# Performance work log

Hardware: AMD Instinct MI355X
Metric: run time of the kernel (lower is better)

The kernel has to match this reference:

```python
import jax, jax.numpy as jnp
import numpy as np

CV_CHAN = 49  # displacement channels; radius = (CV_CHAN - 1) // 2 = 24


def conv1x1(x, W, b):
    # x: [B,C,H,Wd], W: [O,C], b: [O] -> [B,O,H,Wd]
    return jnp.einsum('oc,bchw->bohw', W, x) + b[None, :, None, None]


def corr_volume(f1, f2, radius, eps):
    """Shift-and-dot correlation along width. f1,f2: [B,C,H,W] -> [B,2r+1,H,W].
    Channel k corresponds to displacement d = k - radius; out-of-range positions are 0
    (handled by zero-padding, matching the torch zero-filled shifted tensors)."""
    f1n = f1 / (jnp.linalg.norm(f1, axis=1, keepdims=True) + eps)
    f2n = f2 / (jnp.linalg.norm(f2, axis=1, keepdims=True) + eps)
    Wd = f1.shape[3]
    pad = jnp.pad(f2n, ((0, 0), (0, 0), (0, 0), (radius, radius)))
    # shifted_k[x] = f2n[x - d] = pad[x + 2*radius - k]
    slices = [
        jnp.sum(f1n * jax.lax.dynamic_slice_in_dim(pad, 2 * radius - k, Wd, axis=3), axis=1)
        for k in range(2 * radius + 1)
    ]
    return jnp.stack(slices, axis=1)


def setup_inputs() -> dict:
    key = jax.random.key(0)
    ks = jax.random.split(key, 10)
    B, C, H, W = 4, 128, 128, 256
    F = 128  # fmap channels
    G = 96   # geo encoder output channels
    s = 0.05
    return {
        'feat_l1': jax.random.normal(ks[0], (B, C, H, W), jnp.float32),
        'feat_r1': jax.random.normal(ks[1], (B, C, H, W), jnp.float32),
        'cv0': jax.random.normal(ks[2], (B, CV_CHAN, H, W), jnp.float32),
        'cv1': jax.random.normal(ks[3], (B, CV_CHAN, H, W), jnp.float32),
        'cv2': jax.random.normal(ks[4], (B, CV_CHAN, H, W), jnp.float32),
        'W_f1': jax.random.normal(ks[5], (F, C), jnp.float32) * s,
        'b_f1': jnp.zeros((F,), jnp.float32),
        'W_f2': jax.random.normal(ks[6], (F, C), jnp.float32) * s,
        'b_f2': jnp.zeros((F,), jnp.float32),
        'W_geo': jax.random.normal(ks[7], (G, CV_CHAN), jnp.float32) * s,
        'b_geo': jnp.zeros((G,), jnp.float32),
        'W_sel': jax.random.normal(ks[8], (3, 3 * G), jnp.float32) * s,
        'b_sel': jnp.zeros((3,), jnp.float32),
    }


def reference(feat_l1, feat_r1, cv0, cv1, cv2,
              W_f1, b_f1, W_f2, b_f2, W_geo, b_geo, W_sel, b_sel):
    # init feature maps (init_fmap1 / init_fmap2 as 1x1 convs)
    fmap1 = conv1x1(feat_l1, W_f1, b_f1)
    fmap2 = conv1x1(feat_r1, W_f2, b_f2)
    radius = (CV_CHAN - 1) // 2
    init_corr = corr_volume(fmap1, fmap2, radius, 1e-8)  # [B, CV_CHAN, H, W]

    # geo_volume2 (1x1 conv CV_CHAN -> 96) applied to each geometric volume
    g0 = conv1x1(cv0, W_geo, b_geo)
    g1 = conv1x1(cv1, W_geo, b_geo)
    g2 = conv1x1(cv2, W_geo, b_geo)
    combined_g = jnp.concatenate([g0, g1, g2], axis=1)  # [B, 288, H, W]

    logits = conv1x1(combined_g, W_sel, b_sel)           # [B, 3, H, W]
    w = jax.nn.softmax(logits, axis=1)

    weighted = (w[:, 0:1] * cv0[:, :CV_CHAN]
                + w[:, 1:2] * cv1[:, :CV_CHAN]
                + w[:, 2:3] * cv2[:, :CV_CHAN])
    final = init_corr + weighted
    return (final, init_corr, w)
```

## Files before the change

### kernel.cpp

```cpp
#include <hip/hip_runtime.h>

#define HW 32768
#define WIDTH 256

typedef float f32x4 __attribute__((ext_vector_type(4)));
typedef short s16x8 __attribute__((ext_vector_type(8)));

__device__ __forceinline__ unsigned short f2bf(float f){
    unsigned int u = __float_as_uint(f);
    u += 0x7FFFu + ((u >> 16) & 1u);
    return (unsigned short)(u >> 16);
}
__device__ __forceinline__ unsigned int pk2(float a, float b){
    return (unsigned int)f2bf(a) | ((unsigned int)f2bf(b) << 16);
}

__global__ __launch_bounds__(256, 2) void k_fused(
    const float* __restrict__ fl, const float* __restrict__ fr,
    const float* __restrict__ W1, const float* __restrict__ W2,
    const float* __restrict__ b1, const float* __restrict__ b2,
    float* __restrict__ ic)
{
    __shared__ char pool[67584];
    __shared__ float s1[256], s2[256];
    unsigned short* Wlds = (unsigned short*)pool;
    unsigned short* f2s  = (unsigned short*)pool;
    float* G             = (float*)pool;

    const int blk  = blockIdx.x;
    const int b    = blk >> 7;
    const int h    = blk & 127;
    const int tid  = threadIdx.x;
    const int wv   = tid >> 6;
    const int lane = tid & 63;
    const int quad = lane >> 4;
    const int l15  = lane & 15;

    const float* feats[2] = { fl + (size_t)b * 128 * HW + h * WIDTH,
                              fr + (size_t)b * 128 * HW + h * WIDTH };
    const float* Wms[2]   = { W1, W2 };
    const float* bss[2]   = { b1, b2 };

    unsigned int f1p[64];

    #pragma unroll 1
    for (int F = 0; F < 2; ++F){
        const float* featB = feats[F];
        const float* Wm    = Wms[F];
        const float* bias  = bss[F];

        __syncthreads();
        {
            const int r = tid >> 1, c0 = (tid & 1) * 64;
            #pragma unroll
            for (int i = 0; i < 16; ++i){
                f32x4 v = *(const f32x4*)(Wm + r * 128 + c0 + i * 4);
                uint2 p; p.x = pk2(v[0], v[1]); p.y = pk2(v[2], v[3]);
                *(uint2*)&Wlds[r * 132 + c0 + i * 4] = p;
            }
        }
        __syncthreads();

        f32x4 acc[8][4];
        #pragma unroll
        for (int m = 0; m < 8; ++m)
            #pragma unroll
            for (int nt = 0; nt < 4; ++nt)
                acc[m][nt] = (f32x4){0.f, 0.f, 0.f, 0.f};

        float cur[8], nxt[8];
        {
            const float* bp = featB + (size_t)(quad * 8) * HW + wv * 64 + l15;
            #pragma unroll
            for (int j = 0; j < 8; ++j) cur[j] = bp[(size_t)j * HW];
        }

        #pragma unroll
        for (int kk = 0; kk < 4; ++kk){
            s16x8 af[8];
            #pragma unroll
            for (int m = 0; m < 8; ++m){
                const int base = (m * 16 + l15) * 132 + kk * 32 + quad * 8;
                union { uint2 q2[2]; s16x8 v; } r;
                r.q2[0] = *(const uint2*)&Wlds[base];
                r.q2[1] = *(const uint2*)&Wlds[base + 4];
                af[m] = r.v;
            }
            #pragma unroll
            for (int nt = 0; nt < 4; ++nt){
                const int kn  = kk + ((nt + 1) >> 2);
                const int ntn = (nt + 1) & 3;
                if (kn < 4){
                    const float* bp = featB + (size_t)(kn * 32 + quad * 8) * HW
                                      + wv * 64 + ntn * 16 + l15;
                    #pragma unroll
                    for (int j = 0; j < 8; ++j) nxt[j] = bp[(size_t)j * HW];
                }
                union { unsigned int u[4]; s16x8 v; } rb;
                rb.u[0] = pk2(cur[0], cur[1]); rb.u[1] = pk2(cur[2], cur[3]);
                rb.u[2] = pk2(cur[4], cur[5]); rb.u[3] = pk2(cur[6], cur[7]);
                #pragma unroll
                for (int m = 0; m < 8; ++m)
                    acc[m][nt] = __builtin_amdgcn_mfma_f32_16x16x32_bf16(af[m], rb.v, acc[m][nt], 0, 0, 0);
                #pragma unroll
                for (int j = 0; j < 8; ++j) cur[j] = nxt[j];
            }
        }

        float inv[4];
        #pragma unroll
        for (int nt = 0; nt < 4; ++nt){
            #pragma unroll
            for (int m = 0; m < 8; ++m)
                acc[m][nt] += *(const f32x4*)(bias + m * 16 + quad * 4);
            float n2 = 0.f;
            #pragma unroll
            for (int m = 0; m < 8; ++m)
                #pragma unroll
                for (int r = 0; r < 4; ++r)
                    n2 += acc[m][nt][r] * acc[m][nt][r];
            n2 += __shfl_xor(n2, 16, 64);
            n2 += __shfl_xor(n2, 32, 64);
            inv[nt] = 1.f / (sqrtf(n2) + 1e-8f);
        }

        if (F == 0){
            #pragma unroll
            for (int m = 0; m < 8; ++m)
                #pragma unroll
                for (int nt = 0; nt < 4; ++nt){
                    f1p[m * 8 + nt * 2 + 0] = pk2(acc[m][nt][0], acc[m][nt][1]);
                    f1p[m * 8 + nt * 2 + 1] = pk2(acc[m][nt][2], acc[m][nt][3]);
                }
            if (quad == 0){
                #pragma unroll
                for (int nt = 0; nt < 4; ++nt) s1[wv * 64 + nt * 16 + l15] = inv[nt];
            }
        } else {
            if (quad == 0){
                #pragma unroll
                for (int nt = 0; nt < 4; ++nt) s2[wv * 64 + nt * 16 + l15] = inv[nt];
            }
            __syncthreads();
            #pragma unroll
            for (int nt = 0; nt < 4; ++nt){
                const int px = wv * 64 + nt * 16 + l15;
                #pragma unroll
                for (int m = 0; m < 8; ++m){
                    uint2 p;
                    p.x = pk2(acc[m][nt][0], acc[m][nt][1]);
                    p.y = pk2(acc[m][nt][2], acc[m][nt][3]);
                    *(uint2*)&f2s[px * 132 + m * 16 + quad * 4] = p;
                }
            }
        }
    }
    __syncthreads();

    f32x4 acc_c[4][4];
    #pragma unroll
    for (int st = 0; st < 4; ++st)
        #pragma unroll
        for (int ct = 0; ct < 4; ++ct)
            acc_c[st][ct] = (f32x4){0.f, 0.f, 0.f, 0.f};

    #pragma unroll
    for (int st = 0; st < 4; ++st){
        s16x8 afc[4];
        #pragma unroll
        for (int kk = 0; kk < 4; ++kk){
            union { unsigned int u[4]; s16x8 v; } r;
            #pragma unroll
            for (int j2 = 0; j2 < 4; ++j2){
                const int rp  = j2 & 1;
                const int qs  = (quad & 1) * 2 + (j2 >> 1);
                const int src = qs * 16 + l15;
                unsigned int a0 = (unsigned int)__shfl((int)f1p[(kk * 2 + 0) * 8 + st * 2 + rp], src, 64);
                unsigned int a1 = (unsigned int)__shfl((int)f1p[(kk * 2 + 1) * 8 + st * 2 + rp], src, 64);
                r.u[j2] = (quad >> 1) ? a1 : a0;
            }
            afc[kk] = r.v;
        }
        #pragma unroll
        for (int ct = 0; ct < 4; ++ct){
            const int s = wv * 64 + st * 16 + ct * 16 + l15 - 24;
            const bool valid = (s >= 0) && (s < WIDTH);
            const int sc = valid ? s : 0;
            #pragma unroll
            for (int kk = 0; kk < 4; ++kk){
                union { uint2 q2[2]; s16x8 v; } rb;
                rb.q2[0] = *(const uint2*)&f2s[sc * 132 + kk * 32 + quad * 8];
                rb.q2[1] = *(const uint2*)&f2s[sc * 132 + kk * 32 + quad * 8 + 4];
                s16x8 bf = rb.v;
                if (!valid) bf = (s16x8){0,0,0,0,0,0,0,0};
                acc_c[st][ct] = __builtin_amdgcn_mfma_f32_16x16x32_bf16(afc[kk], bf, acc_c[st][ct], 0, 0, 0);
            }
        }
    }
    __syncthreads();
    #pragma unroll
    for (int st = 0; st < 4; ++st)
        #pragma unroll
        for (int ct = 0; ct < 4; ++ct)
            #pragma unroll
            for (int r = 0; r < 4; ++r)
                G[((wv * 4 + st) * 16 + quad * 4 + r) * 66 + ct * 16 + l15] = acc_c[st][ct][r];
    __syncthreads();

    float* obase = ic + (size_t)b * 49 * HW + (size_t)h * WIDTH;
    #pragma unroll
    for (int st = 0; st < 4; ++st){
        const int gx = wv * 64 + st * 16;
        const float sc1 = s1[gx + l15];
        const float* Grow = &G[((wv * 4 + st) * 16 + l15) * 66];
        #pragma unroll
        for (int i = 0; i < 13; ++i){
            const int dd = quad + i * 4;
            if (dd < 49){
                int s2i = gx + l15 + 24 - dd;
                s2i = s2i < 0 ? 0 : (s2i > 255 ? 255 : s2i);
                const float v = Grow[l15 + 48 - dd] * sc1 * s2[s2i];
                obase[(size_t)dd * HW + gx + l15] = v;
            }
        }
    }
}

__global__ void k_prep(const float* __restrict__ Wsel, const float* __restrict__ bsel,
                       const float* __restrict__ Wgeo, const float* __restrict__ bgeo,
                       float* __restrict__ M, float* __restrict__ c0)
{
    int u = threadIdx.x;
    if (u < 441){
        int s = u / 147; int r = u % 147; int i = r / 49; int k = r % 49;
        float acc = 0.f;
        for (int o = 0; o < 96; ++o)
            acc += Wsel[s * 288 + i * 96 + o] * Wgeo[o * 49 + k];
        M[u] = acc;
    } else if (u < 444){
        int s = u - 441;
        float acc = bsel[s];
        for (int i = 0; i < 3; ++i)
            for (int o = 0; o < 96; ++o)
                acc += Wsel[s * 288 + i * 96 + o] * bgeo[o];
        c0[s] = acc;
    }
}

__global__ __launch_bounds__(256, 2) void k_sel(
    const float* __restrict__ cv0, const float* __restrict__ cv1, const float* __restrict__ cv2,
    const float* __restrict__ M, const float* __restrict__ c0,
    const float* __restrict__ ic,
    float* __restrict__ finalO, float* __restrict__ wO)
{
    __shared__ float Ms[441];
    __shared__ float c0s[3];
    const int tid = threadIdx.x;
    for (int i = tid; i < 441; i += 256) Ms[i] = M[i];
    if (tid < 3) c0s[tid] = c0[tid];
    __syncthreads();

    const int gid = blockIdx.x * 256 + tid;
    const int b = gid >> 15;
    const int p = gid & 32767;
    const size_t base = (size_t)b * 49 * HW + p;

    float a0[49], a1[49], a2[49];
    #pragma unroll
    for (int k = 0; k < 49; ++k){
        size_t o = base + (size_t)k * HW;
        a0[k] = cv0[o]; a1[k] = cv1[o]; a2[k] = cv2[o];
    }

    float lg0 = c0s[0], lg1 = c0s[1], lg2 = c0s[2];
    #pragma unroll
    for (int k = 0; k < 49; ++k){
        lg0 += Ms[k]       * a0[k] + Ms[49  + k] * a1[k] + Ms[98  + k] * a2[k];
        lg1 += Ms[147 + k] * a0[k] + Ms[196 + k] * a1[k] + Ms[245 + k] * a2[k];
        lg2 += Ms[294 + k] * a0[k] + Ms[343 + k] * a1[k] + Ms[392 + k] * a2[k];
    }
    float mx = fmaxf(lg0, fmaxf(lg1, lg2));
    float e0 = expf(lg0 - mx), e1 = expf(lg1 - mx), e2 = expf(lg2 - mx);
    float inv = 1.f / (e0 + e1 + e2);
    float w0 = e0 * inv, w1 = e1 * inv, w2 = e2 * inv;

    const size_t wbase = (size_t)b * 3 * HW + p;
    wO[wbase]          = w0;
    wO[wbase + HW]     = w1;
    wO[wbase + 2 * HW] = w2;

    #pragma unroll
    for (int k = 0; k < 49; ++k){
        size_t o = base + (size_t)k * HW;
        finalO[o] = ic[o] + w0 * a0[k] + w1 * a1[k] + w2 * a2[k];
    }
}

extern "C" void kernel_launch(void* const* d_in, const int* in_sizes, int n_in,
                              void* d_out, int out_size, void* d_ws, size_t ws_size,
                              hipStream_t stream)
{
    const float* feat_l1 = (const float*)d_in[0];
    const float* feat_r1 = (const float*)d_in[1];
    const float* cv0     = (const float*)d_in[2];
    const float* cv1     = (const float*)d_in[3];
    const float* cv2     = (const float*)d_in[4];
    const float* W_f1    = (const float*)d_in[5];
    const float* b_f1    = (const float*)d_in[6];
    const float* W_f2    = (const float*)d_in[7];
    const float* b_f2    = (const float*)d_in[8];
    const float* W_geo   = (const float*)d_in[9];
    const float* b_geo   = (const float*)d_in[10];
    const float* W_sel   = (const float*)d_in[11];
    const float* b_sel   = (const float*)d_in[12];

    float* finalO = (float*)d_out;
    float* icO    = (float*)d_out + 6422528;
    float* wO     = (float*)d_out + 12845056;

    float* Mbuf  = (float*)d_ws;
    float* c0buf = Mbuf + 441;

    k_prep<<<1, 512, 0, stream>>>(W_sel, b_sel, W_geo, b_geo, Mbuf, c0buf);
    k_fused<<<512, 256, 0, stream>>>(feat_l1, feat_r1, W_f1, W_f2, b_f1, b_f2, icO);
    k_sel<<<512, 256, 0, stream>>>(cv0, cv1, cv2, Mbuf, c0buf, icO, finalO, wO);
}
```

Baseline: 281.0 us.

## Pre-pack bf16 MFMA weight fragments globally and deepen feature load prefetch

A new small kernel converts both 1x1 conv weight matrices to bf16 once, laid out in MFMA A-fragment order in workspace. The fused kernel now loads these fragments straight from global/L2 instead of staging weights through LDS, which removes two syncthreads pairs and the per-block conversion. Feature loads move from single to double-depth prefetch with a 3-slot ring. The right-image projection now runs first so its LDS store needs no extra barrier. This adds an extra launch and per-lane global weight reads that depend on cache hits.

Measured after the change: 276.1 us. About the same (-1.7%).

```diff
diff --git a/kernel.cpp b/kernel.cpp
--- a/kernel.cpp
+++ b/kernel.cpp
@@ -15,17 +15,32 @@
     return (unsigned int)f2bf(a) | ((unsigned int)f2bf(b) << 16);
 }
 
+__global__ void k_wconv(const float* __restrict__ W1, const float* __restrict__ W2,
+                        unsigned int* __restrict__ Wb)
+{
+    const int pi = blockIdx.x * 256 + threadIdx.x;
+    const int j2   = pi & 3;
+    const int l15  = (pi >> 2) & 15;
+    const int quad = (pi >> 6) & 3;
+    const int m    = (pi >> 8) & 7;
+    const int kk   = (pi >> 11) & 3;
+    const int F    = (pi >> 13) & 1;
+    const float* Wm = F ? W2 : W1;
+    const int row = m * 16 + l15;
+    const int ch  = kk * 32 + quad * 8 + j2 * 2;
+    Wb[pi] = pk2(Wm[row * 128 + ch], Wm[row * 128 + ch + 1]);
+}
+
 __global__ __launch_bounds__(256, 2) void k_fused(
     const float* __restrict__ fl, const float* __restrict__ fr,
-    const float* __restrict__ W1, const float* __restrict__ W2,
+    const unsigned int* __restrict__ Wbu,
     const float* __restrict__ b1, const float* __restrict__ b2,
     float* __restrict__ ic)
 {
-    __shared__ char pool[67584];
+    __shared__ __align__(16) char pool[67584];
     __shared__ float s1[256], s2[256];
-    unsigned short* Wlds = (unsigned short*)pool;
-    unsigned short* f2s  = (unsigned short*)pool;
-    float* G             = (float*)pool;
+    unsigned short* f2s = (unsigned short*)pool;
+    float* G            = (float*)pool;
 
     const int blk  = blockIdx.x;
     const int b    = blk >> 7;
@@ -38,28 +53,16 @@
 
     const float* feats[2] = { fl + (size_t)b * 128 * HW + h * WIDTH,
                               fr + (size_t)b * 128 * HW + h * WIDTH };
-    const float* Wms[2]   = { W1, W2 };
     const float* bss[2]   = { b1, b2 };
 
     unsigned int f1p[64];
 
     #pragma unroll 1
-    for (int F = 0; F < 2; ++F){
+    for (int Fi = 0; Fi < 2; ++Fi){
+        const int F = 1 - Fi;
         const float* featB = feats[F];
-        const float* Wm    = Wms[F];
         const float* bias  = bss[F];
-
-        __syncthreads();
-        {
-            const int r = tid >> 1, c0 = (tid & 1) * 64;
-            #pragma unroll
-            for (int i = 0; i < 16; ++i){
-                f32x4 v = *(const f32x4*)(Wm + r * 128 + c0 + i * 4);
-                uint2 p; p.x = pk2(v[0], v[1]); p.y = pk2(v[2], v[3]);
-                *(uint2*)&Wlds[r * 132 + c0 + i * 4] = p;
-            }
-        }
-        __syncthreads();
+        const unsigned int* WbF = Wbu + F * 8192;
 
         f32x4 acc[8][4];
         #pragma unroll
@@ -68,42 +71,38 @@
             for (int nt = 0; nt < 4; ++nt)
                 acc[m][nt] = (f32x4){0.f, 0.f, 0.f, 0.f};
 
-        float cur[8], nxt[8];
-        {
-            const float* bp = featB + (size_t)(quad * 8) * HW + wv * 64 + l15;
-            #pragma unroll
-            for (int j = 0; j < 8; ++j) cur[j] = bp[(size_t)j * HW];
+        float buf[3][8];
+        #pragma unroll
+        for (int t = 0; t < 2; ++t){
+            const float* bp = featB + (size_t)(quad * 8) * HW + wv * 64 + t * 16 + l15;
+            #pragma unroll
+            for (int j = 0; j < 8; ++j) buf[t][j] = bp[(size_t)j * HW];
         }
 
         #pragma unroll
         for (int kk = 0; kk < 4; ++kk){
             s16x8 af[8];
             #pragma unroll
-            for (int m = 0; m < 8; ++m){
-                const int base = (m * 16 + l15) * 132 + kk * 32 + quad * 8;
-                union { uint2 q2[2]; s16x8 v; } r;
-                r.q2[0] = *(const uint2*)&Wlds[base];
-                r.q2[1] = *(const uint2*)&Wlds[base + 4];
-                af[m] = r.v;
-            }
+            for (int m = 0; m < 8; ++m)
+                af[m] = *(const s16x8*)&WbF[(((kk * 8 + m) * 4 + quad) * 16 + l15) * 4];
+
             #pragma unroll
             for (int nt = 0; nt < 4; ++nt){
-                const int kn  = kk + ((nt + 1) >> 2);
-                const int ntn = (nt + 1) & 3;
-                if (kn < 4){
-                    const float* bp = featB + (size_t)(kn * 32 + quad * 8) * HW
-                                      + wv * 64 + ntn * 16 + l15;
+                const int t = kk * 4 + nt;
+                if (t + 2 < 16){
+                    const int kk2 = (t + 2) >> 2, nt2 = (t + 2) & 3;
+                    const float* bp = featB + (size_t)(kk2 * 32 + quad * 8) * HW
+                                      + wv * 64 + nt2 * 16 + l15;
                     #pragma unroll
-                    for (int j = 0; j < 8; ++j) nxt[j] = bp[(size_t)j * HW];
+                    for (int j = 0; j < 8; ++j) buf[(t + 2) % 3][j] = bp[(size_t)j * HW];
                 }
+                const float* cur = buf[t % 3];
                 union { unsigned int u[4]; s16x8 v; } rb;
                 rb.u[0] = pk2(cur[0], cur[1]); rb.u[1] = pk2(cur[2], cur[3]);
                 rb.u[2] = pk2(cur[4], cur[5]); rb.u[3] = pk2(cur[6], cur[7]);
                 #pragma unroll
                 for (int m = 0; m < 8; ++m)
                     acc[m][nt] = __builtin_amdgcn_mfma_f32_16x16x32_bf16(af[m], rb.v, acc[m][nt], 0, 0, 0);
-                #pragma unroll
-                for (int j = 0; j < 8; ++j) cur[j] = nxt[j];
             }
         }
 
@@ -124,24 +123,11 @@
             inv[nt] = 1.f / (sqrtf(n2) + 1e-8f);
         }
 
-        if (F == 0){
-            #pragma unroll
-            for (int m = 0; m < 8; ++m)
-                #pragma unroll
-                for (int nt = 0; nt < 4; ++nt){
-                    f1p[m * 8 + nt * 2 + 0] = pk2(acc[m][nt][0], acc[m][nt][1]);
-                    f1p[m * 8 + nt * 2 + 1] = pk2(acc[m][nt][2], acc[m][nt][3]);
-                }
+        if (F == 1){
             if (quad == 0){
                 #pragma unroll
-                for (int nt = 0; nt < 4; ++nt) s1[wv * 64 + nt * 16 + l15] = inv[nt];
-            }
-        } else {
-            if (quad == 0){
-                #pragma unroll
                 for (int nt = 0; nt < 4; ++nt) s2[wv * 64 + nt * 16 + l15] = inv[nt];
             }
-            __syncthreads();
             #pragma unroll
             for (int nt = 0; nt < 4; ++nt){
                 const int px = wv * 64 + nt * 16 + l15;
@@ -152,6 +138,18 @@
                     p.y = pk2(acc[m][nt][2], acc[m][nt][3]);
                     *(uint2*)&f2s[px * 132 + m * 16 + quad * 4] = p;
                 }
+            }
+        } else {
+            #pragma unroll
+            for (int m = 0; m < 8; ++m)
+                #pragma unroll
+                for (int nt = 0; nt < 4; ++nt){
+                    f1p[m * 8 + nt * 2 + 0] = pk2(acc[m][nt][0], acc[m][nt][1]);
+                    f1p[m * 8 + nt * 2 + 1] = pk2(acc[m][nt][2], acc[m][nt][3]);
+                }
+            if (quad == 0){
+                #pragma unroll
+                for (int nt = 0; nt < 4; ++nt) s1[wv * 64 + nt * 16 + l15] = inv[nt];
             }
         }
     }
@@ -318,10 +316,12 @@
     float* icO    = (float*)d_out + 6422528;
     float* wO     = (float*)d_out + 12845056;
 
-    float* Mbuf  = (float*)d_ws;
+    unsigned int* Wb = (unsigned int*)d_ws;
+    float* Mbuf  = (float*)((char*)d_ws + 65536);
     float* c0buf = Mbuf + 441;
 
+    k_wconv<<<64, 256, 0, stream>>>(W_f1, W_f2, Wb);
     k_prep<<<1, 512, 0, stream>>>(W_sel, b_sel, W_geo, b_geo, Mbuf, c0buf);
-    k_fused<<<512, 256, 0, stream>>>(feat_l1, feat_r1, W_f1, W_f2, b_f1, b_f2, icO);
+    k_fused<<<512, 256, 0, stream>>>(feat_l1, feat_r1, Wb, b_f1, b_f2, icO);
     k_sel<<<512, 256, 0, stream>>>(cv0, cv1, cv2, Mbuf, c0buf, icO, finalO, wO);
 }
```
